# Optimization experiments

Measured on AMD Instinct MI355X. Metric: run time of the kernel, lower is better.

Reference implementation:

```python
import jax, jax.numpy as jnp
import numpy as np

B, S, D, H = 4, 2048, 768, 12


def setup_inputs() -> dict:
    key = jax.random.key(0)
    k1, k2, k3, k4 = jax.random.split(key, 4)
    std = D ** (-0.5)
    x = jax.random.normal(k1, (B, S, D), dtype=jnp.float32)
    W_QKV = jax.random.normal(k2, (3, D, D), dtype=jnp.float32) * std
    W_O = jax.random.normal(k3, (D, D), dtype=jnp.float32) * std
    token_positions = jnp.sort(jax.random.randint(k4, (B, S), 0, S), axis=-1).astype(jnp.int64)
    return {"x": x, "W_QKV": W_QKV, "W_O": W_O, "token_positions": token_positions,
            "num_heads": H, "theta": 10000}


def _apply_rope(t, cos, sin):
    # t: (B, H, S, Hd); cos/sin: (B, 1, S, Hd/2). Interleaved even/odd pairs.
    te, to = t[..., 0::2], t[..., 1::2]
    re = te * cos - to * sin
    ro = te * sin + to * cos
    return jnp.stack([re, ro], axis=-1).reshape(t.shape)


def reference(x, W_QKV, W_O, token_positions, num_heads, theta):
    b, s, d = x.shape
    hd = d // num_heads  # d_head = d_k = d_v
    # fused QKV projection: Q = x @ W_QKV[0].T etc.
    qkv = jnp.einsum('bsd,kod->kbso', x, W_QKV)              # (3, B, S, D)
    qkv = qkv.reshape(3, b, s, num_heads, hd).transpose(0, 1, 3, 2, 4)  # (3, B, H, S, Hd)
    q, k, v = qkv[0], qkv[1], qkv[2]
    # RoPE angles: pos * theta^(-2j/d_k)
    inv_freq = jnp.asarray(theta, x.dtype) ** (-(jnp.arange(0, hd, 2, dtype=x.dtype) / hd))
    angles = token_positions.astype(x.dtype)[..., None] * inv_freq    # (B, S, Hd/2)
    cos = jnp.cos(angles)[:, None]                                     # (B, 1, S, Hd/2)
    sin = jnp.sin(angles)[:, None]
    q = _apply_rope(q, cos, sin)
    k = _apply_rope(k, cos, sin)
    # causal attention
    scores = jnp.einsum('bhqd,bhkd->bhqk', q, k) / (hd ** 0.5)        # (B, H, S, S)
    causal = jnp.tril(jnp.ones((s, s), dtype=bool))
    scores = jnp.where(causal, scores, -jnp.inf)
    probs = jax.nn.softmax(scores, axis=-1)
    out = jnp.einsum('bhqk,bhkd->bhqd', probs, v)                      # (B, H, S, Hd)
    out = out.transpose(0, 2, 1, 3).reshape(b, s, d)
    return out @ W_O.T
```

## Files before the change

kernel.cpp:

```cpp
#include <hip/hip_runtime.h>
#include <hip/hip_bf16.h>

typedef __bf16 bf16;
typedef __bf16 bf16x8 __attribute__((ext_vector_type(8)));
typedef __bf16 bf16x4 __attribute__((ext_vector_type(4)));
typedef short  s16x4  __attribute__((ext_vector_type(4)));
typedef float  f32x4  __attribute__((ext_vector_type(4)));

#if defined(__has_builtin)
#if __has_builtin(__builtin_amdgcn_mfma_f32_16x16x16bf16_1k)
#define HAVE_MFMA16 1
#endif
#if __has_builtin(__builtin_amdgcn_exp2f)
#define EXP2(x) __builtin_amdgcn_exp2f(x)
#else
#define EXP2(x) exp2f(x)
#endif
#else
#define EXP2(x) exp2f(x)
#endif

__device__ __forceinline__ void gl_lds16(const void* g, void* l) {
  __builtin_amdgcn_global_load_lds(
      (__attribute__((address_space(1))) const void*)g,
      (__attribute__((address_space(3))) void*)l, 16, 0, 0);
}

__device__ __forceinline__ f32x4 mfma32(bf16x8 a, bf16x8 b, f32x4 c) {
  return __builtin_amdgcn_mfma_f32_16x16x32_bf16(a, b, c, 0, 0, 0);
}
#if HAVE_MFMA16
__device__ __forceinline__ f32x4 mfma16(s16x4 a, s16x4 b, f32x4 c) {
  return __builtin_amdgcn_mfma_f32_16x16x16bf16_1k(a, b, c, 0, 0, 0);
}
#endif

__global__ void cvt3(const float* __restrict__ a, bf16* __restrict__ da,
                     const float* __restrict__ b, bf16* __restrict__ db,
                     const float* __restrict__ c, bf16* __restrict__ dc) {
  int bx = blockIdx.x;
  const float* s; bf16* d; int i;
  if (bx < 6144)      { s = a; d = da; i = bx * 256 + threadIdx.x; }
  else if (bx < 7872) { s = b; d = db; i = (bx - 6144) * 256 + threadIdx.x; }
  else                { s = c; d = dc; i = (bx - 7872) * 256 + threadIdx.x; }
  float4 v = ((const float4*)s)[i];
  bf16x4 o;
  o[0] = (bf16)v.x; o[1] = (bf16)v.y; o[2] = (bf16)v.z; o[3] = (bf16)v.w;
  ((bf16x4*)d)[i] = o;
}

template <int MODE>
__global__ void gemm_bt(const bf16* __restrict__ A, const bf16* __restrict__ Bm,
                        void* __restrict__ Cout, bf16* __restrict__ Vout) {
  constexpr int K = 768;
  __shared__ __align__(16) char As[2][128 * 64];
  __shared__ __align__(16) char Bs[2][128 * 64];
  const int tid = threadIdx.x;
  const int w = tid >> 6, lane = tid & 63;
  const int quad = lane >> 4, l15 = lane & 15;
  const int wrow = w >> 1, wcol = w & 1;
  const int m0 = blockIdx.x * 128, n0 = blockIdx.y * 128;

  f32x4 acc[4][4];
#pragma unroll
  for (int mt = 0; mt < 4; ++mt)
#pragma unroll
    for (int nt = 0; nt < 4; ++nt) acc[mt][nt] = (f32x4){0.f, 0.f, 0.f, 0.f};

  auto stage = [&](int k0, int bufi) {
#pragma unroll
    for (int i = 0; i < 2; ++i) {
      int L = i * 256 + tid;
      int r = L >> 2, cl = L & 3;
      int cg = cl ^ ((r >> 1) & 3);
      gl_lds16(A + (size_t)(m0 + r) * K + k0 + cg * 8, As[bufi] + (i * 256 + w * 64) * 16);
      gl_lds16(Bm + (size_t)(n0 + r) * K + k0 + cg * 8, Bs[bufi] + (i * 256 + w * 64) * 16);
    }
  };

  stage(0, 0);
  int buf = 0;

  for (int k0 = 0; k0 < K; k0 += 32) {
    __syncthreads();
    if (k0 + 32 < K) stage(k0 + 32, buf ^ 1);
    const char* Ab = As[buf];
    const char* Bb = Bs[buf];

    bf16x8 af[4], bfr[4];
#pragma unroll
    for (int mt = 0; mt < 4; ++mt) {
      int r = wrow * 64 + mt * 16 + l15;
      int cl = quad ^ ((r >> 1) & 3);
      af[mt] = *(const bf16x8*)(Ab + r * 64 + cl * 16);
    }
#pragma unroll
    for (int nt = 0; nt < 4; ++nt) {
      int r = wcol * 64 + nt * 16 + l15;
      int cl = quad ^ ((r >> 1) & 3);
      bfr[nt] = *(const bf16x8*)(Bb + r * 64 + cl * 16);
    }
#pragma unroll
    for (int mt = 0; mt < 4; ++mt)
#pragma unroll
      for (int nt = 0; nt < 4; ++nt)
        acc[mt][nt] = mfma32(af[mt], bfr[nt], acc[mt][nt]);
    buf ^= 1;
  }

#pragma unroll
  for (int mt = 0; mt < 4; ++mt)
#pragma unroll
    for (int nt = 0; nt < 4; ++nt)
#pragma unroll
      for (int r = 0; r < 4; ++r) {
        int m = m0 + wrow * 64 + mt * 16 + quad * 4 + r;
        int n = n0 + wcol * 64 + nt * 16 + l15;
        float v = acc[mt][nt][r];
        if (MODE == 0) {
          ((float*)Cout)[(size_t)m * 768 + n] = v;
        } else {
          int mat = n / 768, rem = n % 768;
          int hh = rem >> 6, d = rem & 63;
          int bb = m >> 11, s = m & 2047;
          if (mat == 2)
            Vout[(((size_t)(bb * 12 + hh) * 64 + d) * 2048) + s] = (bf16)v;
          else
            ((bf16*)Cout)[(((size_t)(mat * 4 + bb) * 12 + hh) * 2048 + s) * 64 + d] = (bf16)v;
        }
      }
}

__global__ void rope_k(bf16* __restrict__ qk, const int* __restrict__ tpos,
                       const int* __restrict__ thetap) {
  int i = blockIdx.x * 256 + threadIdx.x;
  int d2 = i & 31;
  int s = (i >> 5) & 2047;
  int rest = i >> 16;
  int rb = rest / 12;
  int b = rb & 3;
  size_t off = ((size_t)rest * 2048 + s) * 64 + d2 * 2;
  int pos = tpos[b * 2048 + s];
  float lt = log2f((float)(*thetap));
  float fr = exp2f(-(float)d2 * (1.0f / 32.0f) * lt);
  float ang = (float)pos * fr;
  float sn, cs;
  sincosf(ang, &sn, &cs);
  float scq = (rest < 48) ? 0.18033688011112042f : 1.0f;
  float te = (float)qk[off], to = (float)qk[off + 1];
  qk[off]     = (bf16)((te * cs - to * sn) * scq);
  qk[off + 1] = (bf16)((te * sn + to * cs) * scq);
}

__global__ __launch_bounds__(128, 3)
void attn(const bf16* __restrict__ qkv, const bf16* __restrict__ vt,
          bf16* __restrict__ aout) {
  const int bx = blockIdx.x;
  const int qt = 31 - (bx / 48);
  const int bh = bx % 48;
  const int b = bh / 12, h = bh % 12;
  const int tid = threadIdx.x, w = tid >> 6, lane = tid & 63;
  const int quad = lane >> 4, l15 = lane & 15;
  const bf16* Q  = qkv + (size_t)bh * (2048 * 64);
  const bf16* Kp = qkv + (size_t)(48 + bh) * (2048 * 64);
  const bf16* Vt = vt + (size_t)bh * (64 * 2048);
  __shared__ __align__(16) char Ks[2][64 * 128];
  __shared__ __align__(16) char Vs[2][64 * 128];

  const int qbase = qt * 64 + w * 32;
  bf16x8 qf[2][2];
#pragma unroll
  for (int j = 0; j < 2; ++j) {
    qf[j][0] = *(const bf16x8*)(Q + (size_t)(qbase + j * 16 + l15) * 64 + quad * 8);
    qf[j][1] = *(const bf16x8*)(Q + (size_t)(qbase + j * 16 + l15) * 64 + 32 + quad * 8);
  }

  float li[2] = {0.f, 0.f};
  f32x4 o[2][4];
#pragma unroll
  for (int j = 0; j < 2; ++j)
#pragma unroll
    for (int dt = 0; dt < 4; ++dt) o[j][dt] = (f32x4){0.f, 0.f, 0.f, 0.f};

  auto stage = [&](int kb, int bufi) {
#pragma unroll
    for (int i = 0; i < 4; ++i) {
      int L = i * 128 + tid;
      int r = L >> 3, cl = L & 7, cg = cl ^ (r & 7);
      gl_lds16(Kp + (size_t)(kb * 64 + r) * 64 + cg * 8, Ks[bufi] + L * 16);
      gl_lds16(Vt + (size_t)r * 2048 + kb * 64 + cg * 8, Vs[bufi] + L * 16);
    }
  };

  stage(0, 0);
  int buf = 0;

  for (int kb = 0; kb <= qt; ++kb) {
    __syncthreads();
    if (kb < qt) stage(kb + 1, buf ^ 1);
    const char* Kb = Ks[buf];
    const char* Vb = Vs[buf];

    float S[2][16];
#pragma unroll
    for (int sk = 0; sk < 4; ++sk) {
      int r = sk * 16 + l15;
      int cl0 = quad ^ (r & 7);
      int cl1 = (4 + quad) ^ (r & 7);
      bf16x8 kf0 = *(const bf16x8*)(Kb + r * 128 + cl0 * 16);
      bf16x8 kf1 = *(const bf16x8*)(Kb + r * 128 + cl1 * 16);
#pragma unroll
      for (int j = 0; j < 2; ++j) {
        f32x4 st = (f32x4){0.f, 0.f, 0.f, 0.f};
        st = mfma32(kf0, qf[j][0], st);
        st = mfma32(kf1, qf[j][1], st);
#pragma unroll
        for (int rr = 0; rr < 4; ++rr) S[j][sk * 4 + rr] = st[rr];
      }
    }
    if (kb == qt) {
#pragma unroll
      for (int j = 0; j < 2; ++j)
#pragma unroll
        for (int sk = 0; sk < 4; ++sk)
#pragma unroll
          for (int rr = 0; rr < 4; ++rr) {
            int key = kb * 64 + sk * 16 + quad * 4 + rr;
            if (key > qbase + j * 16 + l15) S[j][sk * 4 + rr] = -1e30f;
          }
    }

#if HAVE_MFMA16
    s16x4 pf[2][4];
#endif
#pragma unroll
    for (int j = 0; j < 2; ++j) {
      float rs = 0.f;
#pragma unroll
      for (int sk = 0; sk < 4; ++sk) {
        bf16x4 pb;
#pragma unroll
        for (int rr = 0; rr < 4; ++rr) {
          float p = EXP2(S[j][sk * 4 + rr]);
          rs += p;
          pb[rr] = (bf16)p;
#if !HAVE_MFMA16
          S[j][sk * 4 + rr] = p;
#endif
        }
#if HAVE_MFMA16
        pf[j][sk] = __builtin_bit_cast(s16x4, pb);
#else
        (void)pb;
#endif
      }
      rs += __shfl_xor(rs, 16);
      rs += __shfl_xor(rs, 32);
      li[j] += rs;
    }

#if HAVE_MFMA16
#pragma unroll
    for (int sk = 0; sk < 4; ++sk)
#pragma unroll
      for (int dt = 0; dt < 4; ++dt) {
        int rr = dt * 16 + l15;
        int c = sk * 2 + (quad >> 1);
        int cl = c ^ (rr & 7);
        s16x4 vf = *(const s16x4*)(Vb + rr * 128 + cl * 16 + (quad & 1) * 8);
        o[0][dt] = mfma16(pf[0][sk], vf, o[0][dt]);
        o[1][dt] = mfma16(pf[1][sk], vf, o[1][dt]);
      }
#else
#pragma unroll
    for (int j = 0; j < 2; ++j)
#pragma unroll
      for (int kc = 0; kc < 2; ++kc) {
        bf16x8 af;
#pragma unroll
        for (int jj = 0; jj < 8; ++jj) {
          int sq = (quad & 1) * 2 + (jj >> 2);
          int src = sq * 16 + l15;
          float v0 = __shfl(S[j][kc * 8 + (jj & 3)], src);
          float v1 = __shfl(S[j][kc * 8 + 4 + (jj & 3)], src);
          af[jj] = (bf16)((quad < 2) ? v0 : v1);
        }
#pragma unroll
        for (int dt = 0; dt < 4; ++dt) {
          int rr = dt * 16 + l15;
          int c = kc * 4 + quad;
          int cl = c ^ (rr & 7);
          bf16x8 vf = *(const bf16x8*)(Vb + rr * 128 + cl * 16);
          o[j][dt] = mfma32(af, vf, o[j][dt]);
        }
      }
#endif
    buf ^= 1;
  }

#pragma unroll
  for (int j = 0; j < 2; ++j) {
    float lr[4];
#pragma unroll
    for (int rr = 0; rr < 4; ++rr)
      lr[rr] = __builtin_amdgcn_rcpf(__shfl(li[j], quad * 4 + rr));
#pragma unroll
    for (int dt = 0; dt < 4; ++dt)
#pragma unroll
      for (int rr = 0; rr < 4; ++rr) {
        int q = qbase + j * 16 + quad * 4 + rr;
        int n = h * 64 + dt * 16 + l15;
        aout[((size_t)b * 2048 + q) * 768 + n] = (bf16)(o[j][dt][rr] * lr[rr]);
      }
  }
}

extern "C" void kernel_launch(void* const* d_in, const int* in_sizes, int n_in,
                              void* d_out, int out_size, void* d_ws, size_t ws_size,
                              hipStream_t stream) {
  const float* x    = (const float*)d_in[0];
  const float* wqkv = (const float*)d_in[1];
  const float* wo   = (const float*)d_in[2];
  const int* tpos   = (const int*)d_in[3];
  const int* thetap = (const int*)d_in[5];

  char* ws = (char*)d_ws;
  bf16* xb    = (bf16*)(ws);
  bf16* wqkvb = (bf16*)(ws + 12582912);
  bf16* wob   = (bf16*)(ws + 16121856);
  bf16* qkv   = (bf16*)(ws + 17301504);
  bf16* vtb   = (bf16*)(ws + 55050240);

  cvt3<<<8448, 256, 0, stream>>>(x, xb, wqkv, wqkvb, wo, wob);
  gemm_bt<1><<<dim3(64, 18), 256, 0, stream>>>(xb, wqkvb, (void*)qkv, vtb);
  rope_k<<<24576, 256, 0, stream>>>(qkv, tpos, thetap);
  attn<<<1536, 128, 0, stream>>>(qkv, vtb, xb);
  gemm_bt<0><<<dim3(64, 6), 256, 0, stream>>>(xb, wob, (void*)d_out, nullptr);
}
```

Before: 226.3 us.

## Shrink GEMM tiles to 64x128 with two-wave blocks and vectorize V-transpose stores

```diff
diff --git a/kernel.cpp b/kernel.cpp
--- a/kernel.cpp
+++ b/kernel.cpp
@@ -50,31 +50,37 @@
 }
 
 template <int MODE>
-__global__ void gemm_bt(const bf16* __restrict__ A, const bf16* __restrict__ Bm,
-                        void* __restrict__ Cout, bf16* __restrict__ Vout) {
+__global__ __launch_bounds__(128, 3)
+void gemm_bt(const bf16* __restrict__ A, const bf16* __restrict__ Bm,
+             void* __restrict__ Cout, bf16* __restrict__ Vout) {
   constexpr int K = 768;
-  __shared__ __align__(16) char As[2][128 * 64];
+  __shared__ __align__(16) char As[2][64 * 64];
   __shared__ __align__(16) char Bs[2][128 * 64];
   const int tid = threadIdx.x;
   const int w = tid >> 6, lane = tid & 63;
   const int quad = lane >> 4, l15 = lane & 15;
-  const int wrow = w >> 1, wcol = w & 1;
-  const int m0 = blockIdx.x * 128, n0 = blockIdx.y * 128;
-
-  f32x4 acc[4][4];
-#pragma unroll
-  for (int mt = 0; mt < 4; ++mt)
-#pragma unroll
-    for (int nt = 0; nt < 4; ++nt) acc[mt][nt] = (f32x4){0.f, 0.f, 0.f, 0.f};
+  const int m0 = blockIdx.x * 64, n0 = blockIdx.y * 128;
+
+  f32x4 acc[2][8];
+#pragma unroll
+  for (int mt = 0; mt < 2; ++mt)
+#pragma unroll
+    for (int nt = 0; nt < 8; ++nt) acc[mt][nt] = (f32x4){0.f, 0.f, 0.f, 0.f};
 
   auto stage = [&](int k0, int bufi) {
 #pragma unroll
     for (int i = 0; i < 2; ++i) {
-      int L = i * 256 + tid;
+      int L = i * 128 + tid;
       int r = L >> 2, cl = L & 3;
       int cg = cl ^ ((r >> 1) & 3);
-      gl_lds16(A + (size_t)(m0 + r) * K + k0 + cg * 8, As[bufi] + (i * 256 + w * 64) * 16);
-      gl_lds16(Bm + (size_t)(n0 + r) * K + k0 + cg * 8, Bs[bufi] + (i * 256 + w * 64) * 16);
+      gl_lds16(A + (size_t)(m0 + r) * K + k0 + cg * 8, As[bufi] + L * 16);
+    }
+#pragma unroll
+    for (int i = 0; i < 4; ++i) {
+      int L = i * 128 + tid;
+      int r = L >> 2, cl = L & 3;
+      int cg = cl ^ ((r >> 1) & 3);
+      gl_lds16(Bm + (size_t)(n0 + r) * K + k0 + cg * 8, Bs[bufi] + L * 16);
     }
   };
 
@@ -87,48 +93,51 @@
     const char* Ab = As[buf];
     const char* Bb = Bs[buf];
 
-    bf16x8 af[4], bfr[4];
-#pragma unroll
-    for (int mt = 0; mt < 4; ++mt) {
-      int r = wrow * 64 + mt * 16 + l15;
+    bf16x8 af[2];
+#pragma unroll
+    for (int mt = 0; mt < 2; ++mt) {
+      int r = w * 32 + mt * 16 + l15;
       int cl = quad ^ ((r >> 1) & 3);
       af[mt] = *(const bf16x8*)(Ab + r * 64 + cl * 16);
     }
 #pragma unroll
-    for (int nt = 0; nt < 4; ++nt) {
-      int r = wcol * 64 + nt * 16 + l15;
+    for (int nt = 0; nt < 8; ++nt) {
+      int r = nt * 16 + l15;
       int cl = quad ^ ((r >> 1) & 3);
-      bfr[nt] = *(const bf16x8*)(Bb + r * 64 + cl * 16);
-    }
-#pragma unroll
-    for (int mt = 0; mt < 4; ++mt)
-#pragma unroll
-      for (int nt = 0; nt < 4; ++nt)
-        acc[mt][nt] = mfma32(af[mt], bfr[nt], acc[mt][nt]);
+      bf16x8 bfr = *(const bf16x8*)(Bb + r * 64 + cl * 16);
+      acc[0][nt] = mfma32(af[0], bfr, acc[0][nt]);
+      acc[1][nt] = mfma32(af[1], bfr, acc[1][nt]);
+    }
     buf ^= 1;
   }
 
 #pragma unroll
-  for (int mt = 0; mt < 4; ++mt)
-#pragma unroll
-    for (int nt = 0; nt < 4; ++nt)
-#pragma unroll
-      for (int r = 0; r < 4; ++r) {
-        int m = m0 + wrow * 64 + mt * 16 + quad * 4 + r;
-        int n = n0 + wcol * 64 + nt * 16 + l15;
-        float v = acc[mt][nt][r];
-        if (MODE == 0) {
-          ((float*)Cout)[(size_t)m * 768 + n] = v;
+  for (int mt = 0; mt < 2; ++mt)
+#pragma unroll
+    for (int nt = 0; nt < 8; ++nt) {
+      int n = n0 + nt * 16 + l15;
+      int mb = m0 + w * 32 + mt * 16 + quad * 4;
+      if (MODE == 0) {
+#pragma unroll
+        for (int r = 0; r < 4; ++r)
+          ((float*)Cout)[(size_t)(mb + r) * 768 + n] = acc[mt][nt][r];
+      } else {
+        int mat = n / 768, rem = n % 768;
+        int hh = rem >> 6, d = rem & 63;
+        int bb = mb >> 11, s = mb & 2047;
+        if (mat == 2) {
+          bf16x4 pv;
+#pragma unroll
+          for (int r = 0; r < 4; ++r) pv[r] = (bf16)acc[mt][nt][r];
+          *(bf16x4*)(Vout + (((size_t)(bb * 12 + hh) * 64 + d) * 2048) + s) = pv;
         } else {
-          int mat = n / 768, rem = n % 768;
-          int hh = rem >> 6, d = rem & 63;
-          int bb = m >> 11, s = m & 2047;
-          if (mat == 2)
-            Vout[(((size_t)(bb * 12 + hh) * 64 + d) * 2048) + s] = (bf16)v;
-          else
-            ((bf16*)Cout)[(((size_t)(mat * 4 + bb) * 12 + hh) * 2048 + s) * 64 + d] = (bf16)v;
+#pragma unroll
+          for (int r = 0; r < 4; ++r)
+            ((bf16*)Cout)[(((size_t)(mat * 4 + bb) * 12 + hh) * 2048 + (s + r)) * 64 + d] =
+                (bf16)acc[mt][nt][r];
         }
       }
+    }
 }
 
 __global__ void rope_k(bf16* __restrict__ qk, const int* __restrict__ tpos,
@@ -332,8 +341,8 @@
   bf16* vtb   = (bf16*)(ws + 55050240);
 
   cvt3<<<8448, 256, 0, stream>>>(x, xb, wqkv, wqkvb, wo, wob);
-  gemm_bt<1><<<dim3(64, 18), 256, 0, stream>>>(xb, wqkvb, (void*)qkv, vtb);
+  gemm_bt<1><<<dim3(128, 18), 128, 0, stream>>>(xb, wqkvb, (void*)qkv, vtb);
   rope_k<<<24576, 256, 0, stream>>>(qkv, tpos, thetap);
   attn<<<1536, 128, 0, stream>>>(qkv, vtb, xb);
-  gemm_bt<0><<<dim3(64, 6), 256, 0, stream>>>(xb, wob, (void*)d_out, nullptr);
-}
+  gemm_bt<0><<<dim3(128, 6), 128, 0, stream>>>(xb, wob, (void*)d_out, nullptr);
+}
```

Result: slower. 236.0 us (+4.3%).
